# Optimization experiments

Hardware: AMD Instinct MI355X
Metric: run time of the kernel (lower is better)

The kernel has to match this reference:

```python
import jax, jax.numpy as jnp
import numpy as np
import math

A = 256            # n_agents == batch rows (epymarl stacks agents along batch)
B = A
OBS = 512          # obs_shape = (input_shape - n_actions) // 2
NA = 64            # n_actions
MSG = 2048         # messages_shape (divisible by A)
H = 1024           # hidden_dim
T = 3              # trajectory_length
TAU = OBS + NA
VD = MSG // A      # per-agent message dim


def setup_inputs() -> dict:
    key = jax.random.key(0)
    keys = iter(jax.random.split(key, 40))
    def lin(o, i):
        w = jax.random.normal(next(keys), (o, i), jnp.float32) * (i ** -0.5)
        return w, jnp.zeros((o,), jnp.float32)
    d = {}
    d["inputs"] = jax.random.normal(next(keys), (B, 2 * OBS + NA + MSG), jnp.float32)
    d["hidden_state"] = jax.random.normal(next(keys), (B, 3 * H), jnp.float32) * 0.1
    for name, o, i in [("pi_fc1", H, OBS + MSG), ("pi_fc2", NA, H),
                       ("fa_fc1", H, OBS), ("fa_fc2", (A - 1) * NA, H),
                       ("fo_fc1", H, NA * A + OBS), ("fo_fc2", OBS, H),
                       ("am_qs", H, MSG), ("am_ks", H, TAU), ("am_vs", VD, TAU)]:
        d[name + "_w"], d[name + "_b"] = lin(o, i)
    for name in ["pi_rnn", "fa_rnn", "fo_rnn"]:
        d[name + "_wih"], d[name + "_bih"] = lin(3 * H, H)
        d[name + "_whh"], d[name + "_bhh"] = lin(3 * H, H)
    return d


def _gru(x, h, wih, whh, bih, bhh):
    gi = x @ wih.T + bih
    gh = h @ whh.T + bhh
    ir, iz, i_n = jnp.split(gi, 3, -1)
    hr, hz, h_n = jnp.split(gh, 3, -1)
    r = jax.nn.sigmoid(ir + hr)
    z = jax.nn.sigmoid(iz + hz)
    n = jnp.tanh(i_n + r * h_n)
    return (1.0 - z) * n + z * h


def reference(inputs, hidden_state,
              pi_fc1_w, pi_fc1_b, pi_fc2_w, pi_fc2_b,
              pi_rnn_wih, pi_rnn_whh, pi_rnn_bih, pi_rnn_bhh,
              fa_fc1_w, fa_fc1_b, fa_fc2_w, fa_fc2_b,
              fa_rnn_wih, fa_rnn_whh, fa_rnn_bih, fa_rnn_bhh,
              fo_fc1_w, fo_fc1_b, fo_fc2_w, fo_fc2_b,
              fo_rnn_wih, fo_rnn_whh, fo_rnn_bih, fo_rnn_bhh,
              am_qs_w, am_qs_b, am_ks_w, am_ks_b, am_vs_w, am_vs_b):
    sg = jax.lax.stop_gradient
    lin = lambda x, w, b: x @ w.T + b
    h_fa = hidden_state[:, :H]
    h_fo = hidden_state[:, H:2 * H]
    h_pi0 = hidden_state[:, -H:]
    obs = inputs[:, :OBS]
    prev_obs = inputs[:, OBS:2 * OBS]
    prev_act = sg(inputs[:, 2 * OBS:2 * OBS + NA])   # .detach() in torch
    prev_msg = inputs[:, -MSG:]

    def pi(o, m, h):
        x = jax.nn.relu(lin(jnp.concatenate([o, m], -1), pi_fc1_w, pi_fc1_b))
        h2 = _gru(x, h, pi_rnn_wih, pi_rnn_whh, pi_rnn_bih, pi_rnn_bhh)
        return lin(h2, pi_fc2_w, pi_fc2_b), h2

    # ---- ImaginedTrajectory rollout (fixed small T, python loop is structural) ----
    o, a, h_pi = prev_obs, prev_act, h_pi0
    observations, actions = [o], [a]
    for _ in range(T - 1):
        x = jax.nn.relu(lin(o, fa_fc1_w, fa_fc1_b))
        h_fa = _gru(x, h_fa, fa_rnn_wih, fa_rnn_whh, fa_rnn_bih, fa_rnn_bhh)
        q = lin(h_fa, fa_fc2_w, fa_fc2_b)                       # [B,(A-1)*NA]
        qs = jax.nn.softmax(q.reshape(B, A - 1, NA), -1)
        # torch stack(qs_out).reshape(orig): scrambles (A-1,B) order, kept faithfully
        fa = jnp.transpose(qs, (1, 0, 2)).reshape(B, (A - 1) * NA)
        x2 = jax.nn.relu(lin(jnp.concatenate([fa, a, o], -1), fo_fc1_w, fo_fc1_b))
        h_fo = _gru(x2, h_fo, fo_rnn_wih, fo_rnn_whh, fo_rnn_bih, fo_rnn_bhh)
        nxt_o = lin(h_fo, fo_fc2_w, fo_fc2_b)
        nxt_a, h_pi = pi(sg(o), sg(prev_msg), sg(h_pi))         # forward_pi detaches inputs
        o, a = nxt_o, nxt_a
        observations.append(o)
        actions.append(a)
    taus = jnp.stack([jnp.concatenate([observations[t], actions[t]], -1)
                      for t in range(T)])                        # [T,B,TAU]

    # ---- AttentionMechanism: batched equivalent of the per-agent python loops ----
    # k rows are indexed j*n_agents + i with batch == n_agents, i.e. k[t, b] here.
    qv = lin(prev_msg, am_qs_w, am_qs_b)                         # [B,H]
    kk = jnp.einsum('tbi,hi->tbh', taus, am_ks_w) + am_ks_b      # [T,B,H]
    vv = jnp.einsum('tbi,vi->tbv', taus, am_vs_w) + am_vs_b      # [T,B,VD]
    alpha = jax.nn.softmax(jnp.einsum('bh,tbh->bt', qv, kk) / math.sqrt(H), -1)
    new_message = jnp.einsum('bt,tbv->bv', alpha, vv)            # [B,VD]

    # cat([msg]*A, 0).reshape(B,-1): each agent receives all agents' messages
    pi_msg = jnp.tile(new_message, (A, 1)).reshape(B, -1)        # [B,MSG]
    action, h_pi_f = pi(obs, pi_msg, h_pi0)                      # uses ORIGINAL h_pi slice
    h_out = jnp.concatenate([h_fa, h_fo, h_pi_f], -1)            # [B,3H]
    q_out = jnp.concatenate([new_message, action], -1)           # [B,VD+NA]
    return q_out, h_out
```

## Files before the change

### kernel.cpp

```cpp
#include <hip/hip_runtime.h>
#include <hip/hip_bf16.h>
#include <math.h>

#define OBS 512
#define MSG 2048
#define TAU 576
#define TAUP 640
#define QN 16320
#define X2W 16896
#define INW 3136
#define PIW 2560

typedef short short8v __attribute__((ext_vector_type(8)));
typedef float f32x4 __attribute__((ext_vector_type(4)));
typedef __hip_bfloat16 bf;

__device__ inline unsigned short bfbits(float x) {
  bf h = __float2bfloat16(x);
  return *reinterpret_cast<unsigned short*>(&h);
}

__device__ inline ushort4 cvtf4(float4 v) {
  ushort4 r;
  r.x = bfbits(v.x); r.y = bfbits(v.y); r.z = bfbits(v.z); r.w = bfbits(v.w);
  return r;
}

__device__ inline void gload16(const void* g, void* l) {
  __builtin_amdgcn_global_load_lds((__attribute__((address_space(1))) void*)(g),
                                   (__attribute__((address_space(3))) void*)(l), 16, 0, 0);
}

struct MMSet {
  const bf* A;
  const float* W;
  const float* bias;
  float* C;
  bf* Cb;
  int lda, ldw, ldc, ldcb;
};

template<int ACT, bool ATOMIC, bool DUAL>
__global__ __launch_bounds__(256)
void k_mm(MMSet s0, MMSet s1, int kSteps)
{
  __shared__ bf As[2][64 * 64];
  __shared__ bf Bs[2][64 * 64];
  const MMSet S = (DUAL && blockIdx.z) ? s1 : s0;
  const int tid = threadIdx.x;
  const int lane = tid & 63;
  const int wid = tid >> 6;

  const int gx = gridDim.x, gy = gridDim.y;
  const int nwg = gx * gy;
  const int hw = blockIdx.y * gx + blockIdx.x;
  const int qq = nwg >> 3, rr = nwg & 7;
  const int xcd = hw & 7, idx = hw >> 3;
  const int logical = (xcd < rr) ? xcd * (qq + 1) + idx
                                 : rr * (qq + 1) + (xcd - rr) * qq + idx;
  const int m0 = (logical % gy) * 64;
  const int n0 = (logical / gy) * 64;
  const size_t k0 = ATOMIC ? (size_t)blockIdx.z * kSteps * 64 : 0;

  const bf* Ab = S.A + (size_t)m0 * S.lda + k0;
  const float* Bb = S.W + (size_t)n0 * S.ldw + k0;

  int arow[2], acol[2], adst[2];
#pragma unroll
  for (int r = 0; r < 2; ++r) {
    int chunk = r * 256 + tid;
    arow[r] = chunk >> 3;
    acol[r] = ((chunk & 7) ^ (arow[r] & 7)) * 8;
    adst[r] = chunk * 8;
  }
  int brow[4], bcol[4], bdst[4];
#pragma unroll
  for (int r = 0; r < 4; ++r) {
    int c = r * 256 + tid;
    brow[r] = c >> 4;
    int g = (c & 15) >> 1, half = c & 1;
    bcol[r] = (c & 15) * 4;
    bdst[r] = brow[r] * 64 + ((g ^ (brow[r] & 7)) << 3) + half * 4;
  }

  const int wr = wid >> 1, wc = wid & 1;
  const int fr = lane & 15, q = lane >> 4;
  const int xm = fr & 7;

  f32x4 acc00 = {}, acc01 = {}, acc10 = {}, acc11 = {};
  float4 w0, w1, w2, w3;

  auto stageA = [&](int buf, int kt) {
#pragma unroll
    for (int r = 0; r < 2; ++r)
      gload16(Ab + (size_t)arow[r] * S.lda + kt + acol[r], &As[buf][adst[r]]);
  };
  auto loadB = [&](int kt) {
    w0 = *(const float4*)(Bb + (size_t)brow[0] * S.ldw + kt + bcol[0]);
    w1 = *(const float4*)(Bb + (size_t)brow[1] * S.ldw + kt + bcol[1]);
    w2 = *(const float4*)(Bb + (size_t)brow[2] * S.ldw + kt + bcol[2]);
    w3 = *(const float4*)(Bb + (size_t)brow[3] * S.ldw + kt + bcol[3]);
  };
  auto writeB = [&](int buf) {
    *(ushort4*)&Bs[buf][bdst[0]] = cvtf4(w0);
    *(ushort4*)&Bs[buf][bdst[1]] = cvtf4(w1);
    *(ushort4*)&Bs[buf][bdst[2]] = cvtf4(w2);
    *(ushort4*)&Bs[buf][bdst[3]] = cvtf4(w3);
  };

  stageA(0, 0);
  loadB(0);
  writeB(0);
  __syncthreads();

  for (int t = 0; t < kSteps; ++t) {
    const int buf = t & 1;
    if (t + 1 < kSteps) {
      stageA(buf ^ 1, (t + 1) * 64);
      loadB((t + 1) * 64);
    }
    const bf* Ac = As[buf];
    const bf* Bc = Bs[buf];
#pragma unroll
    for (int ks = 0; ks < 2; ++ks) {
      const int cc = ks * 4 + q;
      const int co = ((cc ^ xm) << 3);
      short8v a0 = *(const short8v*)&Ac[(wr * 32 +  0 + fr) * 64 + co];
      short8v a1 = *(const short8v*)&Ac[(wr * 32 + 16 + fr) * 64 + co];
      short8v b0 = *(const short8v*)&Bc[(wc * 32 +  0 + fr) * 64 + co];
      short8v b1 = *(const short8v*)&Bc[(wc * 32 + 16 + fr) * 64 + co];
      acc00 = __builtin_amdgcn_mfma_f32_16x16x32_bf16(a0, b0, acc00, 0, 0, 0);
      acc01 = __builtin_amdgcn_mfma_f32_16x16x32_bf16(a0, b1, acc01, 0, 0, 0);
      acc10 = __builtin_amdgcn_mfma_f32_16x16x32_bf16(a1, b0, acc10, 0, 0, 0);
      acc11 = __builtin_amdgcn_mfma_f32_16x16x32_bf16(a1, b1, acc11, 0, 0, 0);
    }
    if (t + 1 < kSteps) writeB(buf ^ 1);
    __syncthreads();
  }

  const int mb0 = m0 + wr * 32 + q * 4;
  const int mb1 = mb0 + 16;
  const int nc0 = n0 + wc * 32 + fr;
  const int nc1 = nc0 + 16;
  if (ATOMIC) {
#pragma unroll
    for (int v = 0; v < 4; ++v) {
      atomicAdd(&S.C[(size_t)(mb0 + v) * S.ldc + nc0], acc00[v]);
      atomicAdd(&S.C[(size_t)(mb0 + v) * S.ldc + nc1], acc01[v]);
      atomicAdd(&S.C[(size_t)(mb1 + v) * S.ldc + nc0], acc10[v]);
      atomicAdd(&S.C[(size_t)(mb1 + v) * S.ldc + nc1], acc11[v]);
    }
  } else {
    const float bb0 = S.bias[nc0], bb1 = S.bias[nc1];
#pragma unroll
    for (int v = 0; v < 4; ++v) {
      float v00 = acc00[v] + bb0, v01 = acc01[v] + bb1;
      float v10 = acc10[v] + bb0, v11 = acc11[v] + bb1;
      if (ACT) { v00 = fmaxf(v00, 0.f); v01 = fmaxf(v01, 0.f);
                 v10 = fmaxf(v10, 0.f); v11 = fmaxf(v11, 0.f); }
      if (S.C) {
        S.C[(size_t)(mb0 + v) * S.ldc + nc0] = v00;
        S.C[(size_t)(mb0 + v) * S.ldc + nc1] = v01;
        S.C[(size_t)(mb1 + v) * S.ldc + nc0] = v10;
        S.C[(size_t)(mb1 + v) * S.ldc + nc1] = v11;
      }
      if (S.Cb) {
        S.Cb[(size_t)(mb0 + v) * S.ldcb + nc0] = __float2bfloat16(v00);
        S.Cb[(size_t)(mb0 + v) * S.ldcb + nc1] = __float2bfloat16(v01);
        S.Cb[(size_t)(mb1 + v) * S.ldcb + nc0] = __float2bfloat16(v10);
        S.Cb[(size_t)(mb1 + v) * S.ldcb + nc1] = __float2bfloat16(v11);
      }
    }
  }
}

__global__ __launch_bounds__(256)
void k_init(const float* __restrict__ in, const float* __restrict__ hid,
            float* __restrict__ h32a, float* __restrict__ h32o, float* __restrict__ h32p,
            bf* __restrict__ hba, bf* __restrict__ hbo,
            bf* __restrict__ hbp, bf* __restrict__ hbp0,
            bf* __restrict__ taus, bf* __restrict__ msgb,
            const float* __restrict__ fo1b, float* __restrict__ xf0, float* __restrict__ xf1,
            const float* __restrict__ pi1b, float* __restrict__ xp0,
            float* __restrict__ xp1, float* __restrict__ xp2)
{
  const int bx = blockIdx.x;
  if (bx < 3072) {
    int idx = bx * 256 + threadIdx.x;
    int b = idx / 3072, c = idx % 3072;
    float v = hid[idx];
    bf hb = __float2bfloat16(v);
    int j = c & 1023;
    if (c < 1024)      { h32a[b * 1024 + j] = v; hba[b * 1024 + j] = hb; }
    else if (c < 2048) { h32o[b * 1024 + j] = v; hbo[b * 1024 + j] = hb; }
    else               { h32p[b * 1024 + j] = v; hbp[b * 1024 + j] = hb; hbp0[b * 1024 + j] = hb; }
  } else if (bx < 3072 + 1920) {
    int idx = (bx - 3072) * 256 + threadIdx.x;
    int t = idx / (256 * TAUP);
    int r = (idx / TAUP) % 256;
    int c = idx % TAUP;
    float v = 0.f;
    if (t == 0 && c < TAU)
      v = (c < OBS) ? in[(size_t)r * INW + OBS + c]
                    : in[(size_t)r * INW + 2 * OBS + (c - OBS)];
    taus[idx] = __float2bfloat16(v);
  } else if (bx < 3072 + 1920 + 2048) {
    int idx = (bx - 3072 - 1920) * 256 + threadIdx.x;
    int b = idx >> 11, c = idx & 2047;
    msgb[idx] = __float2bfloat16(in[(size_t)b * INW + 1088 + c]);
  } else if (bx < 3072 + 1920 + 2048 + 1024) {
    int idx = (bx - 3072 - 1920 - 2048) * 256 + threadIdx.x;
    float v = fo1b[idx & 1023];
    xf0[idx] = v; xf1[idx] = v;
  } else {
    int idx = (bx - 3072 - 1920 - 2048 - 1024) * 256 + threadIdx.x;
    float v = pi1b[idx & 1023];
    xp0[idx] = v; xp1[idx] = v; xp2[idx] = v;
  }
}

__global__ __launch_bounds__(256)
void k_gru(const float* __restrict__ gi, const float* __restrict__ gh,
           const float* __restrict__ hs, int ldsrc,
           float* __restrict__ hd, int lddst, bf* __restrict__ hb)
{
  int idx = blockIdx.x * 256 + threadIdx.x;
  int b = idx >> 10, j = idx & 1023;
  float ir = gi[b * 3072 + j];
  float iz = gi[b * 3072 + 1024 + j];
  float in_ = gi[b * 3072 + 2048 + j];
  float hr = gh[b * 3072 + j];
  float hz = gh[b * 3072 + 1024 + j];
  float hn = gh[b * 3072 + 2048 + j];
  float r = 1.f / (1.f + expf(-(ir + hr)));
  float z = 1.f / (1.f + expf(-(iz + hz)));
  float n = tanhf(in_ + r * hn);
  float h = hs[(size_t)b * ldsrc + j];
  float o = (1.f - z) * n + z * h;
  hd[(size_t)b * lddst + j] = o;
  hb[idx] = __float2bfloat16(o);
}

__global__ __launch_bounds__(256)
void k_softmax_scatter(const bf* __restrict__ q, bf* __restrict__ x2)
{
  int wid = blockIdx.x * 4 + (threadIdx.x >> 6);
  int lane = threadIdx.x & 63;
  int b = wid / 255, p = wid % 255;
  float v = __bfloat162float(q[(size_t)b * QN + p * 64 + lane]);
  float m = v;
#pragma unroll
  for (int s = 32; s; s >>= 1) m = fmaxf(m, __shfl_xor(m, s));
  float e = expf(v - m);
  float sum = e;
#pragma unroll
  for (int s = 32; s; s >>= 1) sum += __shfl_xor(sum, s);
  float r = e / sum;
  int flat = p * 16384 + b * 64 + lane;
  int bp = flat / QN;
  int j = flat - bp * QN;
  x2[(size_t)bp * X2W + j] = __float2bfloat16(r);
}

__global__ __launch_bounds__(256)
void k_x2_tail(const bf* __restrict__ taus_t, bf* __restrict__ x2)
{
  int idx = blockIdx.x * 256 + threadIdx.x;
  int b = idx / TAU, c = idx % TAU;
  if (c < 64)
    x2[(size_t)b * X2W + QN + c] = taus_t[(size_t)b * TAUP + OBS + c];
  else
    x2[(size_t)b * X2W + QN + 64 + (c - 64)] = taus_t[(size_t)b * TAUP + (c - 64)];
}

__global__ __launch_bounds__(256)
void k_concat_pi_loop(const bf* __restrict__ taus_t, const bf* __restrict__ msg,
                      bf* __restrict__ piin)
{
  int idx = blockIdx.x * 256 + threadIdx.x;
  int b = idx / PIW, c = idx % PIW;
  piin[idx] = (c < OBS) ? taus_t[(size_t)b * TAUP + c] : msg[b * MSG + (c - OBS)];
}

__global__ __launch_bounds__(256)
void k_concat_pi_final(const float* __restrict__ in, const float* __restrict__ nm,
                       bf* __restrict__ piin)
{
  int idx = blockIdx.x * 256 + threadIdx.x;
  int b = idx / PIW, c = idx % PIW;
  float v = (c < OBS) ? in[(size_t)b * INW + c] : nm[c - OBS];
  piin[idx] = __float2bfloat16(v);
}

__global__ __launch_bounds__(256)
void k_relu_cvt(const float* __restrict__ s, bf* __restrict__ d)
{
  int idx = blockIdx.x * 256 + threadIdx.x;
  d[idx] = __float2bfloat16(fmaxf(s[idx], 0.f));
}

__global__ __launch_bounds__(64)
void k_vv(const bf* __restrict__ taus, const float* __restrict__ w,
          const float* __restrict__ bias, float* __restrict__ vv)
{
  int row = blockIdx.x;
  int lane = threadIdx.x;
  const bf* tr = taus + (size_t)row * TAUP;
  for (int v = 0; v < 8; ++v) {
    float s = 0.f;
    for (int k = lane; k < TAU; k += 64) s += __bfloat162float(tr[k]) * w[v * TAU + k];
#pragma unroll
    for (int d = 32; d; d >>= 1) s += __shfl_xor(s, d);
    if (lane == 0) vv[row * 8 + v] = s + bias[v];
  }
}

__global__ __launch_bounds__(64)
void k_attn(const float* __restrict__ qv, const float* __restrict__ kk,
            const float* __restrict__ vv, float* __restrict__ nm,
            float* __restrict__ out_q)
{
  int b = blockIdx.x;
  int lane = threadIdx.x;
  const float* qb = qv + (size_t)b * 1024;
  float s[3];
#pragma unroll
  for (int t = 0; t < 3; ++t) {
    const float* kb = kk + (size_t)(t * 256 + b) * 1024;
    float acc = 0.f;
    for (int h = lane; h < 1024; h += 64) acc += qb[h] * kb[h];
#pragma unroll
    for (int d = 32; d; d >>= 1) acc += __shfl_xor(acc, d);
    s[t] = acc * (1.f / 32.f);
  }
  float m = fmaxf(s[0], fmaxf(s[1], s[2]));
  float e0 = expf(s[0] - m), e1 = expf(s[1] - m), e2 = expf(s[2] - m);
  float inv = 1.f / (e0 + e1 + e2);
  float a0 = e0 * inv, a1 = e1 * inv, a2 = e2 * inv;
  if (lane < 8) {
    float v = a0 * vv[(0 * 256 + b) * 8 + lane]
            + a1 * vv[(1 * 256 + b) * 8 + lane]
            + a2 * vv[(2 * 256 + b) * 8 + lane];
    nm[b * 8 + lane] = v;
    out_q[b * 72 + lane] = v;
  }
}

__global__ __launch_bounds__(256)
void k_copy_hout(const float* __restrict__ hfa, const float* __restrict__ hfo,
                 float* __restrict__ hout)
{
  int idx = blockIdx.x * 256 + threadIdx.x;
  int b = idx / 2048, c = idx % 2048;
  float v = (c < 1024) ? hfa[b * 1024 + c] : hfo[b * 1024 + (c - 1024)];
  hout[(size_t)b * 3072 + c] = v;
}

extern "C" void kernel_launch(void* const* d_in, const int* in_sizes, int n_in,
                              void* d_out_v, int out_size, void* d_ws, size_t ws_size,
                              hipStream_t stream)
{
  const float* inputs   = (const float*)d_in[0];
  const float* hidden   = (const float*)d_in[1];
  const float* pi_fc1_w = (const float*)d_in[2];
  const float* pi_fc1_b = (const float*)d_in[3];
  const float* pi_fc2_w = (const float*)d_in[4];
  const float* pi_fc2_b = (const float*)d_in[5];
  const float* fa_fc1_w = (const float*)d_in[6];
  const float* fa_fc1_b = (const float*)d_in[7];
  const float* fa_fc2_w = (const float*)d_in[8];
  const float* fa_fc2_b = (const float*)d_in[9];
  const float* fo_fc1_w = (const float*)d_in[10];
  const float* fo_fc1_b = (const float*)d_in[11];
  const float* fo_fc2_w = (const float*)d_in[12];
  const float* fo_fc2_b = (const float*)d_in[13];
  const float* am_qs_w  = (const float*)d_in[14];
  const float* am_qs_b  = (const float*)d_in[15];
  const float* am_ks_w  = (const float*)d_in[16];
  const float* am_ks_b  = (const float*)d_in[17];
  const float* am_vs_w  = (const float*)d_in[18];
  const float* am_vs_b  = (const float*)d_in[19];
  const float* pi_wih   = (const float*)d_in[20];
  const float* pi_bih   = (const float*)d_in[21];
  const float* pi_whh   = (const float*)d_in[22];
  const float* pi_bhh   = (const float*)d_in[23];
  const float* fa_wih   = (const float*)d_in[24];
  const float* fa_bih   = (const float*)d_in[25];
  const float* fa_whh   = (const float*)d_in[26];
  const float* fa_bhh   = (const float*)d_in[27];
  const float* fo_wih   = (const float*)d_in[28];
  const float* fo_bih   = (const float*)d_in[29];
  const float* fo_whh   = (const float*)d_in[30];
  const float* fo_bhh   = (const float*)d_in[31];

  float* out = (float*)d_out_v;
  char* p = (char*)d_ws;
  auto alloc = [&](size_t bytes) { void* r = p; p += (bytes + 255) & ~(size_t)255; return r; };

  bf* HFAB = (bf*)alloc((size_t)256 * 1024 * 2);
  bf* HFOB = (bf*)alloc((size_t)256 * 1024 * 2);
  bf* HPIB = (bf*)alloc((size_t)256 * 1024 * 2);
  bf* HPI0B = (bf*)alloc((size_t)256 * 1024 * 2);
  bf* XBUFB = (bf*)alloc((size_t)256 * 1024 * 2);
  bf* TAUSB = (bf*)alloc((size_t)3 * 256 * TAUP * 2);
  bf* X2B  = (bf*)alloc((size_t)256 * X2W * 2);
  bf* PIINB = (bf*)alloc((size_t)256 * PIW * 2);
  bf* MSGB = (bf*)alloc((size_t)256 * MSG * 2);
  bf* QBUFB = (bf*)alloc((size_t)256 * QN * 2);
  float* HFA32 = (float*)alloc((size_t)256 * 1024 * 4);
  float* HFO32 = (float*)alloc((size_t)256 * 1024 * 4);
  float* HPI32 = (float*)alloc((size_t)256 * 1024 * 4);
  float* XF32A = (float*)alloc((size_t)256 * 1024 * 4);
  float* XF32B = (float*)alloc((size_t)256 * 1024 * 4);
  float* XP32A = (float*)alloc((size_t)256 * 1024 * 4);
  float* XP32B = (float*)alloc((size_t)256 * 1024 * 4);
  float* XP32C = (float*)alloc((size_t)256 * 1024 * 4);
  float* GI = (float*)alloc((size_t)256 * 3072 * 4);
  float* GH = (float*)alloc((size_t)256 * 3072 * 4);
  float* QV = (float*)alloc((size_t)256 * 1024 * 4);
  float* KK = (float*)alloc((size_t)768 * 1024 * 4);
  float* VV = (float*)alloc((size_t)768 * 8 * 4);
  float* NM = (float*)alloc((size_t)2048 * 4);

  auto mset = [&](const bf* A, int lda, const float* W, int ldw, const float* bias,
                  float* C, int ldc, bf* Cb, int ldcb) {
    MMSet s; s.A = A; s.W = W; s.bias = bias; s.C = C; s.Cb = Cb;
    s.lda = lda; s.ldw = ldw; s.ldc = ldc; s.ldcb = ldcb; return s;
  };
  auto mm = [&](MMSet a, int M, int N, int K, int act) {
    dim3 g(N / 64, M / 64, 1);
    if (act) k_mm<1, false, false><<<g, 256, 0, stream>>>(a, a, K / 64);
    else     k_mm<0, false, false><<<g, 256, 0, stream>>>(a, a, K / 64);
  };
  auto mmAtomic = [&](const bf* A, int lda, const float* W, int ldw,
                      float* C, int M, int N, int K, int z) {
    MMSet s = mset(A, lda, W, ldw, nullptr, C, N, nullptr, 0);
    dim3 g(N / 64, M / 64, z);
    k_mm<0, true, false><<<g, 256, 0, stream>>>(s, s, K / (64 * z));
  };
  auto mmDual = [&](MMSet a, MMSet b, int N, int K) {
    dim3 g(N / 64, 4, 2);
    k_mm<0, false, true><<<g, 256, 0, stream>>>(a, b, K / 64);
  };

  k_init<<<3072 + 1920 + 2048 + 1024 + 1024, 256, 0, stream>>>(inputs, hidden,
      HFA32, HFO32, HPI32, HFAB, HFOB, HPIB, HPI0B, TAUSB, MSGB,
      fo_fc1_b, XF32A, XF32B, pi_fc1_b, XP32A, XP32B, XP32C);

  for (int t = 0; t < 2; ++t) {
    bf* taus_t = TAUSB + (size_t)t * 256 * TAUP;
    bf* taus_n = TAUSB + (size_t)(t + 1) * 256 * TAUP;
    float* xf32 = t ? XF32B : XF32A;
    float* xp32 = t ? XP32B : XP32A;
    mm(mset(taus_t, TAUP, fa_fc1_w, 512, fa_fc1_b, nullptr, 0, XBUFB, 1024), 256, 1024, 512, 1);
    mmDual(mset(XBUFB, 1024, fa_wih, 1024, fa_bih, GI, 3072, nullptr, 0),
           mset(HFAB, 1024, fa_whh, 1024, fa_bhh, GH, 3072, nullptr, 0), 3072, 1024);
    k_gru<<<1024, 256, 0, stream>>>(GI, GH, HFA32, 1024, HFA32, 1024, HFAB);
    mm(mset(HFAB, 1024, fa_fc2_w, 1024, fa_fc2_b, nullptr, 0, QBUFB, QN), 256, QN, 1024, 0);
    k_x2_tail<<<576, 256, 0, stream>>>(taus_t, X2B);
    k_softmax_scatter<<<16320, 256, 0, stream>>>(QBUFB, X2B);
    mmAtomic(X2B, X2W, fo_fc1_w, X2W, xf32, 256, 1024, X2W, 12);
    k_relu_cvt<<<1024, 256, 0, stream>>>(xf32, XBUFB);
    mmDual(mset(XBUFB, 1024, fo_wih, 1024, fo_bih, GI, 3072, nullptr, 0),
           mset(HFOB, 1024, fo_whh, 1024, fo_bhh, GH, 3072, nullptr, 0), 3072, 1024);
    k_gru<<<1024, 256, 0, stream>>>(GI, GH, HFO32, 1024, HFO32, 1024, HFOB);
    mm(mset(HFOB, 1024, fo_fc2_w, 1024, fo_fc2_b, nullptr, 0, taus_n, TAUP), 256, 512, 1024, 0);
    k_concat_pi_loop<<<2560, 256, 0, stream>>>(taus_t, MSGB, PIINB);
    mmAtomic(PIINB, PIW, pi_fc1_w, PIW, xp32, 256, 1024, PIW, 4);
    k_relu_cvt<<<1024, 256, 0, stream>>>(xp32, XBUFB);
    mmDual(mset(XBUFB, 1024, pi_wih, 1024, pi_bih, GI, 3072, nullptr, 0),
           mset(HPIB, 1024, pi_whh, 1024, pi_bhh, GH, 3072, nullptr, 0), 3072, 1024);
    k_gru<<<1024, 256, 0, stream>>>(GI, GH, HPI32, 1024, HPI32, 1024, HPIB);
    mm(mset(HPIB, 1024, pi_fc2_w, 1024, pi_fc2_b, nullptr, 0, taus_n + OBS, TAUP), 256, 64, 1024, 0);
  }

  mm(mset(MSGB, MSG, am_qs_w, MSG, am_qs_b, QV, 1024, nullptr, 0), 256, 1024, 2048, 0);
  mm(mset(TAUSB, TAUP, am_ks_w, TAU, am_ks_b, KK, 1024, nullptr, 0), 768, 1024, TAU, 0);
  k_vv<<<768, 64, 0, stream>>>(TAUSB, am_vs_w, am_vs_b, VV);
  k_attn<<<256, 64, 0, stream>>>(QV, KK, VV, NM, out);

  k_concat_pi_final<<<2560, 256, 0, stream>>>(inputs, NM, PIINB);
  mmAtomic(PIINB, PIW, pi_fc1_w, PIW, XP32C, 256, 1024, PIW, 4);
  k_relu_cvt<<<1024, 256, 0, stream>>>(XP32C, XBUFB);
  mmDual(mset(XBUFB, 1024, pi_wih, 1024, pi_bih, GI, 3072, nullptr, 0),
         mset(HPI0B, 1024, pi_whh, 1024, pi_bhh, GH, 3072, nullptr, 0), 3072, 1024);
  k_gru<<<1024, 256, 0, stream>>>(GI, GH, hidden + 2048, 3072,
                                  out + 256 * 72 + 2048, 3072, HPIB);
  mm(mset(HPIB, 1024, pi_fc2_w, 1024, pi_fc2_b, out + 8, 72, nullptr, 0), 256, 64, 1024, 0);
  k_copy_hout<<<2048, 256, 0, stream>>>(HFA32, HFO32, out + 256 * 72);
  (void)in_sizes; (void)n_in; (void)out_size; (void)ws_size;
}
```

Before: 617.6 us.

## Stage B weights in 256-wide K macro-tiles with deeper load prefetch

Adds a MACRO variant of the bf16 MFMA GEMM in which each block loads a 64x256 fp32 weight slab into registers (16 float4 per thread), converts it to bf16 and stores it in LDS once per four 64-wide K steps. The A operand stays double-buffered per 64-step. The aim is more weight loads in flight per thread, to hide global latency on these weight-bandwidth-bound GEMMs. Split-K counts for the atomic GEMMs are changed (12 to 11, 4 to 5) to fit the 256 granularity. The keys GEMM (K=576) stays on the old path. The costs are extra syncthreads per step, higher register pressure and a larger LDS footprint.

```diff
diff --git a/kernel.cpp b/kernel.cpp
--- a/kernel.cpp
+++ b/kernel.cpp
@@ -40,12 +40,13 @@
   int lda, ldw, ldc, ldcb;
 };
 
-template<int ACT, bool ATOMIC, bool DUAL>
+template<int ACT, bool ATOMIC, bool DUAL, bool MACRO>
 __global__ __launch_bounds__(256)
 void k_mm(MMSet s0, MMSet s1, int kSteps)
 {
+  constexpr int BSN = MACRO ? (64 * 256) : (2 * 64 * 64);
   __shared__ bf As[2][64 * 64];
-  __shared__ bf Bs[2][64 * 64];
+  __shared__ bf Bs[BSN];
   const MMSet S = (DUAL && blockIdx.z) ? s1 : s0;
   const int tid = threadIdx.x;
   const int lane = tid & 63;
@@ -60,7 +61,7 @@
                                  : rr * (qq + 1) + (xcd - rr) * qq + idx;
   const int m0 = (logical % gy) * 64;
   const int n0 = (logical / gy) * 64;
-  const size_t k0 = ATOMIC ? (size_t)blockIdx.z * kSteps * 64 : 0;
+  const size_t k0 = ATOMIC ? (size_t)blockIdx.z * kSteps * (MACRO ? 256 : 64) : 0;
 
   const bf* Ab = S.A + (size_t)m0 * S.lda + k0;
   const float* Bb = S.W + (size_t)n0 * S.ldw + k0;
@@ -73,69 +74,121 @@
     acol[r] = ((chunk & 7) ^ (arow[r] & 7)) * 8;
     adst[r] = chunk * 8;
   }
-  int brow[4], bcol[4], bdst[4];
-#pragma unroll
-  for (int r = 0; r < 4; ++r) {
-    int c = r * 256 + tid;
-    brow[r] = c >> 4;
-    int g = (c & 15) >> 1, half = c & 1;
-    bcol[r] = (c & 15) * 4;
-    bdst[r] = brow[r] * 64 + ((g ^ (brow[r] & 7)) << 3) + half * 4;
-  }
-
   const int wr = wid >> 1, wc = wid & 1;
   const int fr = lane & 15, q = lane >> 4;
   const int xm = fr & 7;
 
   f32x4 acc00 = {}, acc01 = {}, acc10 = {}, acc11 = {};
-  float4 w0, w1, w2, w3;
 
   auto stageA = [&](int buf, int kt) {
 #pragma unroll
     for (int r = 0; r < 2; ++r)
       gload16(Ab + (size_t)arow[r] * S.lda + kt + acol[r], &As[buf][adst[r]]);
   };
-  auto loadB = [&](int kt) {
-    w0 = *(const float4*)(Bb + (size_t)brow[0] * S.ldw + kt + bcol[0]);
-    w1 = *(const float4*)(Bb + (size_t)brow[1] * S.ldw + kt + bcol[1]);
-    w2 = *(const float4*)(Bb + (size_t)brow[2] * S.ldw + kt + bcol[2]);
-    w3 = *(const float4*)(Bb + (size_t)brow[3] * S.ldw + kt + bcol[3]);
-  };
-  auto writeB = [&](int buf) {
-    *(ushort4*)&Bs[buf][bdst[0]] = cvtf4(w0);
-    *(ushort4*)&Bs[buf][bdst[1]] = cvtf4(w1);
-    *(ushort4*)&Bs[buf][bdst[2]] = cvtf4(w2);
-    *(ushort4*)&Bs[buf][bdst[3]] = cvtf4(w3);
-  };
-
-  stageA(0, 0);
-  loadB(0);
-  writeB(0);
-  __syncthreads();
-
-  for (int t = 0; t < kSteps; ++t) {
-    const int buf = t & 1;
-    if (t + 1 < kSteps) {
-      stageA(buf ^ 1, (t + 1) * 64);
-      loadB((t + 1) * 64);
+
+  const int ar0 = wr * 32 + fr, ar1 = ar0 + 16;
+  const int br0 = wc * 32 + fr, br1 = br0 + 16;
+
+  if constexpr (MACRO) {
+    float4 wreg[16];
+    const int rw = tid >> 6;
+    const int lb = tid & 63;
+    const int gB = lb >> 1, hB = lb & 1;
+    const int subB = gB >> 3, gloB = gB & 7;
+    auto loadB = [&](int mi) {
+      const float* base = Bb + (size_t)mi * 256 + lb * 4;
+#pragma unroll
+      for (int j = 0; j < 16; ++j)
+        wreg[j] = *(const float4*)(base + (size_t)(j * 4 + rw) * S.ldw);
+    };
+    auto writeB = [&]() {
+#pragma unroll
+      for (int j = 0; j < 16; ++j) {
+        const int r = j * 4 + rw;
+        const int off = r * 256 + (subB * 8 + (gloB ^ (r & 7))) * 8 + hB * 4;
+        *(ushort4*)&Bs[off] = cvtf4(wreg[j]);
+      }
+    };
+    loadB(0);
+    writeB();
+    stageA(0, 0);
+    __syncthreads();
+    const int total = kSteps * 4;
+    for (int m = 0; m < kSteps; ++m) {
+      if (m + 1 < kSteps) loadB(m + 1);
+#pragma unroll
+      for (int s = 0; s < 4; ++s) {
+        const int u = m * 4 + s;
+        if (u + 1 < total) stageA((u + 1) & 1, (u + 1) * 64);
+        const bf* Ac = As[u & 1];
+#pragma unroll
+        for (int ks = 0; ks < 2; ++ks) {
+          const int cc = ks * 4 + q;
+          const int co = ((cc ^ xm) << 3);
+          short8v a0 = *(const short8v*)&Ac[ar0 * 64 + co];
+          short8v a1 = *(const short8v*)&Ac[ar1 * 64 + co];
+          short8v b0 = *(const short8v*)&Bs[br0 * 256 + s * 64 + co];
+          short8v b1 = *(const short8v*)&Bs[br1 * 256 + s * 64 + co];
+          acc00 = __builtin_amdgcn_mfma_f32_16x16x32_bf16(a0, b0, acc00, 0, 0, 0);
+          acc01 = __builtin_amdgcn_mfma_f32_16x16x32_bf16(a0, b1, acc01, 0, 0, 0);
+          acc10 = __builtin_amdgcn_mfma_f32_16x16x32_bf16(a1, b0, acc10, 0, 0, 0);
+          acc11 = __builtin_amdgcn_mfma_f32_16x16x32_bf16(a1, b1, acc11, 0, 0, 0);
+        }
+        __syncthreads();
+      }
+      if (m + 1 < kSteps) { writeB(); __syncthreads(); }
     }
-    const bf* Ac = As[buf];
-    const bf* Bc = Bs[buf];
-#pragma unroll
-    for (int ks = 0; ks < 2; ++ks) {
-      const int cc = ks * 4 + q;
-      const int co = ((cc ^ xm) << 3);
-      short8v a0 = *(const short8v*)&Ac[(wr * 32 +  0 + fr) * 64 + co];
-      short8v a1 = *(const short8v*)&Ac[(wr * 32 + 16 + fr) * 64 + co];
-      short8v b0 = *(const short8v*)&Bc[(wc * 32 +  0 + fr) * 64 + co];
-      short8v b1 = *(const short8v*)&Bc[(wc * 32 + 16 + fr) * 64 + co];
-      acc00 = __builtin_amdgcn_mfma_f32_16x16x32_bf16(a0, b0, acc00, 0, 0, 0);
-      acc01 = __builtin_amdgcn_mfma_f32_16x16x32_bf16(a0, b1, acc01, 0, 0, 0);
-      acc10 = __builtin_amdgcn_mfma_f32_16x16x32_bf16(a1, b0, acc10, 0, 0, 0);
-      acc11 = __builtin_amdgcn_mfma_f32_16x16x32_bf16(a1, b1, acc11, 0, 0, 0);
+  } else {
+    int brow[4], bcol[4], bdst[4];
+#pragma unroll
+    for (int r = 0; r < 4; ++r) {
+      int c = r * 256 + tid;
+      brow[r] = c >> 4;
+      int g = (c & 15) >> 1, half = c & 1;
+      bcol[r] = (c & 15) * 4;
+      bdst[r] = brow[r] * 64 + ((g ^ (brow[r] & 7)) << 3) + half * 4;
     }
-    if (t + 1 < kSteps) writeB(buf ^ 1);
+    float4 w0, w1, w2, w3;
+    auto loadB = [&](int kt) {
+      w0 = *(const float4*)(Bb + (size_t)brow[0] * S.ldw + kt + bcol[0]);
+      w1 = *(const float4*)(Bb + (size_t)brow[1] * S.ldw + kt + bcol[1]);
+      w2 = *(const float4*)(Bb + (size_t)brow[2] * S.ldw + kt + bcol[2]);
+      w3 = *(const float4*)(Bb + (size_t)brow[3] * S.ldw + kt + bcol[3]);
+    };
+    auto writeB = [&](int buf) {
+      *(ushort4*)&Bs[buf * 4096 + bdst[0]] = cvtf4(w0);
+      *(ushort4*)&Bs[buf * 4096 + bdst[1]] = cvtf4(w1);
+      *(ushort4*)&Bs[buf * 4096 + bdst[2]] = cvtf4(w2);
+      *(ushort4*)&Bs[buf * 4096 + bdst[3]] = cvtf4(w3);
+    };
+    stageA(0, 0);
+    loadB(0);
+    writeB(0);
     __syncthreads();
+    for (int t = 0; t < kSteps; ++t) {
+      const int buf = t & 1;
+      if (t + 1 < kSteps) {
+        stageA(buf ^ 1, (t + 1) * 64);
+        loadB((t + 1) * 64);
+      }
+      const bf* Ac = As[buf];
+      const bf* Bc = &Bs[buf * 4096];
+#pragma unroll
+      for (int ks = 0; ks < 2; ++ks) {
+        const int cc = ks * 4 + q;
+        const int co = ((cc ^ xm) << 3);
+        short8v a0 = *(const short8v*)&Ac[ar0 * 64 + co];
+        short8v a1 = *(const short8v*)&Ac[ar1 * 64 + co];
+        short8v b0 = *(const short8v*)&Bc[br0 * 64 + co];
+        short8v b1 = *(const short8v*)&Bc[br1 * 64 + co];
+        acc00 = __builtin_amdgcn_mfma_f32_16x16x32_bf16(a0, b0, acc00, 0, 0, 0);
+        acc01 = __builtin_amdgcn_mfma_f32_16x16x32_bf16(a0, b1, acc01, 0, 0, 0);
+        acc10 = __builtin_amdgcn_mfma_f32_16x16x32_bf16(a1, b0, acc10, 0, 0, 0);
+        acc11 = __builtin_amdgcn_mfma_f32_16x16x32_bf16(a1, b1, acc11, 0, 0, 0);
+      }
+      if (t + 1 < kSteps) writeB(buf ^ 1);
+      __syncthreads();
+    }
   }
 
   const int mb0 = m0 + wr * 32 + q * 4;
@@ -427,20 +480,24 @@
     MMSet s; s.A = A; s.W = W; s.bias = bias; s.C = C; s.Cb = Cb;
     s.lda = lda; s.ldw = ldw; s.ldc = ldc; s.ldcb = ldcb; return s;
   };
-  auto mm = [&](MMSet a, int M, int N, int K, int act) {
+  auto mmM = [&](MMSet a, int M, int N, int K, int act) {
     dim3 g(N / 64, M / 64, 1);
-    if (act) k_mm<1, false, false><<<g, 256, 0, stream>>>(a, a, K / 64);
-    else     k_mm<0, false, false><<<g, 256, 0, stream>>>(a, a, K / 64);
+    if (act) k_mm<1, false, false, true><<<g, 256, 0, stream>>>(a, a, K / 256);
+    else     k_mm<0, false, false, true><<<g, 256, 0, stream>>>(a, a, K / 256);
   };
-  auto mmAtomic = [&](const bf* A, int lda, const float* W, int ldw,
-                      float* C, int M, int N, int K, int z) {
+  auto mmAtomicM = [&](const bf* A, int lda, const float* W, int ldw,
+                       float* C, int M, int N, int K, int z) {
     MMSet s = mset(A, lda, W, ldw, nullptr, C, N, nullptr, 0);
     dim3 g(N / 64, M / 64, z);
-    k_mm<0, true, false><<<g, 256, 0, stream>>>(s, s, K / (64 * z));
+    k_mm<0, true, false, true><<<g, 256, 0, stream>>>(s, s, K / (256 * z));
   };
-  auto mmDual = [&](MMSet a, MMSet b, int N, int K) {
+  auto mmDualM = [&](MMSet a, MMSet b, int N, int K) {
     dim3 g(N / 64, 4, 2);
-    k_mm<0, false, true><<<g, 256, 0, stream>>>(a, b, K / 64);
+    k_mm<0, false, true, true><<<g, 256, 0, stream>>>(a, b, K / 256);
+  };
+  auto mmKS = [&](MMSet a, int M, int N, int K) {
+    dim3 g(N / 64, M / 64, 1);
+    k_mm<0, false, false, false><<<g, 256, 0, stream>>>(a, a, K / 64);
   };
 
   k_init<<<3072 + 1920 + 2048 + 1024 + 1024, 256, 0, stream>>>(inputs, hidden,
@@ -452,41 +509,41 @@
     bf* taus_n = TAUSB + (size_t)(t + 1) * 256 * TAUP;
     float* xf32 = t ? XF32B : XF32A;
     float* xp32 = t ? XP32B : XP32A;
-    mm(mset(taus_t, TAUP, fa_fc1_w, 512, fa_fc1_b, nullptr, 0, XBUFB, 1024), 256, 1024, 512, 1);
-    mmDual(mset(XBUFB, 1024, fa_wih, 1024, fa_bih, GI, 3072, nullptr, 0),
-           mset(HFAB, 1024, fa_whh, 1024, fa_bhh, GH, 3072, nullptr, 0), 3072, 1024);
+    mmM(mset(taus_t, TAUP, fa_fc1_w, 512, fa_fc1_b, nullptr, 0, XBUFB, 1024), 256, 1024, 512, 1);
+    mmDualM(mset(XBUFB, 1024, fa_wih, 1024, fa_bih, GI, 3072, nullptr, 0),
+            mset(HFAB, 1024, fa_whh, 1024, fa_bhh, GH, 3072, nullptr, 0), 3072, 1024);
     k_gru<<<1024, 256, 0, stream>>>(GI, GH, HFA32, 1024, HFA32, 1024, HFAB);
-    mm(mset(HFAB, 1024, fa_fc2_w, 1024, fa_fc2_b, nullptr, 0, QBUFB, QN), 256, QN, 1024, 0);
+    mmM(mset(HFAB, 1024, fa_fc2_w, 1024, fa_fc2_b, nullptr, 0, QBUFB, QN), 256, QN, 1024, 0);
     k_x2_tail<<<576, 256, 0, stream>>>(taus_t, X2B);
     k_softmax_scatter<<<16320, 256, 0, stream>>>(QBUFB, X2B);
-    mmAtomic(X2B, X2W, fo_fc1_w, X2W, xf32, 256, 1024, X2W, 12);
+    mmAtomicM(X2B, X2W, fo_fc1_w, X2W, xf32, 256, 1024, X2W, 11);
     k_relu_cvt<<<1024, 256, 0, stream>>>(xf32, XBUFB);
-    mmDual(mset(XBUFB, 1024, fo_wih, 1024, fo_bih, GI, 3072, nullptr, 0),
-           mset(HFOB, 1024, fo_whh, 1024, fo_bhh, GH, 3072, nullptr, 0), 3072, 1024);
+    mmDualM(mset(XBUFB, 1024, fo_wih, 1024, fo_bih, GI, 3072, nullptr, 0),
+            mset(HFOB, 1024, fo_whh, 1024, fo_bhh, GH, 3072, nullptr, 0), 3072, 1024);
     k_gru<<<1024, 256, 0, stream>>>(GI, GH, HFO32, 1024, HFO32, 1024, HFOB);
-    mm(mset(HFOB, 1024, fo_fc2_w, 1024, fo_fc2_b, nullptr, 0, taus_n, TAUP), 256, 512, 1024, 0);
+    mmM(mset(HFOB, 1024, fo_fc2_w, 1024, fo_fc2_b, nullptr, 0, taus_n, TAUP), 256, 512, 1024, 0);
     k_concat_pi_loop<<<2560, 256, 0, stream>>>(taus_t, MSGB, PIINB);
-    mmAtomic(PIINB, PIW, pi_fc1_w, PIW, xp32, 256, 1024, PIW, 4);
+    mmAtomicM(PIINB, PIW, pi_fc1_w, PIW, xp32, 256, 1024, PIW, 5);
     k_relu_cvt<<<1024, 256, 0, stream>>>(xp32, XBUFB);
-    mmDual(mset(XBUFB, 1024, pi_wih, 1024, pi_bih, GI, 3072, nullptr, 0),
-           mset(HPIB, 1024, pi_whh, 1024, pi_bhh, GH, 3072, nullptr, 0), 3072, 1024);
+    mmDualM(mset(XBUFB, 1024, pi_wih, 1024, pi_bih, GI, 3072, nullptr, 0),
+            mset(HPIB, 1024, pi_whh, 1024, pi_bhh, GH, 3072, nullptr, 0), 3072, 1024);
     k_gru<<<1024, 256, 0, stream>>>(GI, GH, HPI32, 1024, HPI32, 1024, HPIB);
-    mm(mset(HPIB, 1024, pi_fc2_w, 1024, pi_fc2_b, nullptr, 0, taus_n + OBS, TAUP), 256, 64, 1024, 0);
-  }
-
-  mm(mset(MSGB, MSG, am_qs_w, MSG, am_qs_b, QV, 1024, nullptr, 0), 256, 1024, 2048, 0);
-  mm(mset(TAUSB, TAUP, am_ks_w, TAU, am_ks_b, KK, 1024, nullptr, 0), 768, 1024, TAU, 0);
+    mmM(mset(HPIB, 1024, pi_fc2_w, 1024, pi_fc2_b, nullptr, 0, taus_n + OBS, TAUP), 256, 64, 1024, 0);
+  }
+
+  mmM(mset(MSGB, MSG, am_qs_w, MSG, am_qs_b, QV, 1024, nullptr, 0), 256, 1024, 2048, 0);
+  mmKS(mset(TAUSB, TAUP, am_ks_w, TAU, am_ks_b, KK, 1024, nullptr, 0), 768, 1024, 576);
   k_vv<<<768, 64, 0, stream>>>(TAUSB, am_vs_w, am_vs_b, VV);
   k_attn<<<256, 64, 0, stream>>>(QV, KK, VV, NM, out);
 
   k_concat_pi_final<<<2560, 256, 0, stream>>>(inputs, NM, PIINB);
-  mmAtomic(PIINB, PIW, pi_fc1_w, PIW, XP32C, 256, 1024, PIW, 4);
+  mmAtomicM(PIINB, PIW, pi_fc1_w, PIW, XP32C, 256, 1024, PIW, 5);
   k_relu_cvt<<<1024, 256, 0, stream>>>(XP32C, XBUFB);
-  mmDual(mset(XBUFB, 1024, pi_wih, 1024, pi_bih, GI, 3072, nullptr, 0),
-         mset(HPI0B, 1024, pi_whh, 1024, pi_bhh, GH, 3072, nullptr, 0), 3072, 1024);
+  mmDualM(mset(XBUFB, 1024, pi_wih, 1024, pi_bih, GI, 3072, nullptr, 0),
+          mset(HPI0B, 1024, pi_whh, 1024, pi_bhh, GH, 3072, nullptr, 0), 3072, 1024);
   k_gru<<<1024, 256, 0, stream>>>(GI, GH, hidden + 2048, 3072,
                                   out + 256 * 72 + 2048, 3072, HPIB);
-  mm(mset(HPIB, 1024, pi_fc2_w, 1024, pi_fc2_b, out + 8, 72, nullptr, 0), 256, 64, 1024, 0);
+  mmM(mset(HPIB, 1024, pi_fc2_w, 1024, pi_fc2_b, out + 8, 72, nullptr, 0), 256, 64, 1024, 0);
   k_copy_hout<<<2048, 256, 0, stream>>>(HFA32, HFO32, out + 256 * 72);
   (void)in_sizes; (void)n_in; (void)out_size; (void)ws_size;
 }
```

Result: no change. 628.1 us (+1.7%).

## Add full-M 256x128 GEMM kernel for fp32-weight layers so weights stream once

Applied to the files above, without the earlier changes.

Adds a new 512-thread GEMM kernel whose block covers all 256 rows and 128 columns, so each fp32 weight row is loaded and converted to bf16 only once rather than once per 64-row M tile. The large fa_fc2, fo_fc1 and pi_fc1 projections use it, with split-K atomics for the fc1 layers; fo_fc1 split changed from 12 to 8. The am_qs projection moves to the start as a split-K atomic GEMM, with its bias preloaded in the init kernel. Tradeoff: fewer blocks, so lower parallelism on skinny layers, and higher register and LDS use per block.

```diff
diff --git a/kernel.cpp b/kernel.cpp
--- a/kernel.cpp
+++ b/kernel.cpp
@@ -174,6 +174,117 @@
   }
 }
 
+template<int ACT, bool ATOMIC>
+__global__ __launch_bounds__(512)
+void k_mm2(MMSet S, int kSteps, int Nw, int Nlim)
+{
+  __shared__ bf As[2][256 * 32];
+  __shared__ bf Bs[2][128 * 32];
+  const int tid = threadIdx.x;
+  const int lane = tid & 63;
+  const int wid = tid >> 6;
+  const int n0 = blockIdx.x * 128;
+  const size_t k0 = (size_t)blockIdx.z * kSteps * 32;
+
+  const bf* Ab = S.A + k0;
+
+  int arow[2], acol[2], adst[2];
+#pragma unroll
+  for (int r = 0; r < 2; ++r) {
+    int c = r * 512 + tid;
+    arow[r] = c >> 2;
+    acol[r] = ((c & 3) ^ (arow[r] & 3)) * 8;
+    adst[r] = c * 8;
+  }
+  const float* bsrc[2];
+  int bdst[2];
+#pragma unroll
+  for (int r = 0; r < 2; ++r) {
+    int c = r * 512 + tid;
+    int row = c >> 3, f4 = c & 7;
+    int rowg = n0 + row; if (rowg >= Nw) rowg = Nw - 1;
+    bsrc[r] = S.W + (size_t)rowg * S.ldw + k0 + f4 * 4;
+    bdst[r] = row * 32 + (((f4 >> 1) ^ (row & 3)) << 3) + (f4 & 1) * 4;
+  }
+
+  const int wr = wid & 3, wc = wid >> 2;
+  const int fr = lane & 15, q = lane >> 4;
+
+  f32x4 acc[4][4] = {};
+  float4 w0, w1;
+
+  auto stageA = [&](int buf, int kt) {
+#pragma unroll
+    for (int r = 0; r < 2; ++r)
+      gload16(Ab + (size_t)arow[r] * S.lda + kt + acol[r], &As[buf][adst[r]]);
+  };
+  auto loadB = [&](int kt) {
+    w0 = *(const float4*)(bsrc[0] + kt);
+    w1 = *(const float4*)(bsrc[1] + kt);
+  };
+  auto writeB = [&](int buf) {
+    *(ushort4*)&Bs[buf][bdst[0]] = cvtf4(w0);
+    *(ushort4*)&Bs[buf][bdst[1]] = cvtf4(w1);
+  };
+
+  stageA(0, 0);
+  loadB(0);
+  writeB(0);
+  __syncthreads();
+
+  for (int t = 0; t < kSteps; ++t) {
+    const int buf = t & 1;
+    if (t + 1 < kSteps) {
+      stageA(buf ^ 1, (t + 1) * 32);
+      loadB((t + 1) * 32);
+    }
+    const bf* Ac = As[buf];
+    const bf* Bc = Bs[buf];
+    short8v af[4], bfv[4];
+#pragma unroll
+    for (int i = 0; i < 4; ++i) {
+      const int ar = wr * 64 + i * 16 + fr;
+      af[i] = *(const short8v*)&Ac[ar * 32 + ((q ^ (ar & 3)) << 3)];
+    }
+#pragma unroll
+    for (int j = 0; j < 4; ++j) {
+      const int br = wc * 64 + j * 16 + fr;
+      bfv[j] = *(const short8v*)&Bc[br * 32 + ((q ^ (br & 3)) << 3)];
+    }
+#pragma unroll
+    for (int i = 0; i < 4; ++i)
+#pragma unroll
+      for (int j = 0; j < 4; ++j)
+        acc[i][j] = __builtin_amdgcn_mfma_f32_16x16x32_bf16(af[i], bfv[j], acc[i][j], 0, 0, 0);
+    if (t + 1 < kSteps) writeB(buf ^ 1);
+    __syncthreads();
+  }
+
+#pragma unroll
+  for (int i = 0; i < 4; ++i) {
+    const int mb = wr * 64 + i * 16 + q * 4;
+#pragma unroll
+    for (int j = 0; j < 4; ++j) {
+      const int n = n0 + wc * 64 + j * 16 + fr;
+      if (n >= Nlim) continue;
+      if (ATOMIC) {
+#pragma unroll
+        for (int v = 0; v < 4; ++v)
+          atomicAdd(&S.C[(size_t)(mb + v) * S.ldc + n], acc[i][j][v]);
+      } else {
+        const float bb = S.bias[n];
+#pragma unroll
+        for (int v = 0; v < 4; ++v) {
+          float val = acc[i][j][v] + bb;
+          if (ACT) val = fmaxf(val, 0.f);
+          if (S.C)  S.C[(size_t)(mb + v) * S.ldc + n] = val;
+          if (S.Cb) S.Cb[(size_t)(mb + v) * S.ldcb + n] = __float2bfloat16(val);
+        }
+      }
+    }
+  }
+}
+
 __global__ __launch_bounds__(256)
 void k_init(const float* __restrict__ in, const float* __restrict__ hid,
             float* __restrict__ h32a, float* __restrict__ h32o, float* __restrict__ h32p,
@@ -182,7 +293,8 @@
             bf* __restrict__ taus, bf* __restrict__ msgb,
             const float* __restrict__ fo1b, float* __restrict__ xf0, float* __restrict__ xf1,
             const float* __restrict__ pi1b, float* __restrict__ xp0,
-            float* __restrict__ xp1, float* __restrict__ xp2)
+            float* __restrict__ xp1, float* __restrict__ xp2,
+            const float* __restrict__ qsb, float* __restrict__ qv)
 {
   const int bx = blockIdx.x;
   if (bx < 3072) {
@@ -212,10 +324,13 @@
     int idx = (bx - 3072 - 1920 - 2048) * 256 + threadIdx.x;
     float v = fo1b[idx & 1023];
     xf0[idx] = v; xf1[idx] = v;
-  } else {
+  } else if (bx < 3072 + 1920 + 2048 + 2048) {
     int idx = (bx - 3072 - 1920 - 2048 - 1024) * 256 + threadIdx.x;
     float v = pi1b[idx & 1023];
     xp0[idx] = v; xp1[idx] = v; xp2[idx] = v;
+  } else {
+    int idx = (bx - 3072 - 1920 - 2048 - 2048) * 256 + threadIdx.x;
+    qv[idx] = qsb[idx & 1023];
   }
 }
 
@@ -432,20 +547,26 @@
     if (act) k_mm<1, false, false><<<g, 256, 0, stream>>>(a, a, K / 64);
     else     k_mm<0, false, false><<<g, 256, 0, stream>>>(a, a, K / 64);
   };
-  auto mmAtomic = [&](const bf* A, int lda, const float* W, int ldw,
-                      float* C, int M, int N, int K, int z) {
-    MMSet s = mset(A, lda, W, ldw, nullptr, C, N, nullptr, 0);
-    dim3 g(N / 64, M / 64, z);
-    k_mm<0, true, false><<<g, 256, 0, stream>>>(s, s, K / (64 * z));
-  };
   auto mmDual = [&](MMSet a, MMSet b, int N, int K) {
     dim3 g(N / 64, 4, 2);
     k_mm<0, false, true><<<g, 256, 0, stream>>>(a, b, K / 64);
   };
-
-  k_init<<<3072 + 1920 + 2048 + 1024 + 1024, 256, 0, stream>>>(inputs, hidden,
+  auto mm2 = [&](MMSet a, int Npad, int Nw, int Nlim, int K) {
+    dim3 g(Npad / 128, 1, 1);
+    k_mm2<0, false><<<g, 512, 0, stream>>>(a, K / 32, Nw, Nlim);
+  };
+  auto mm2Atomic = [&](const bf* A, int lda, const float* W, int ldw,
+                       float* C, int N, int K, int z) {
+    MMSet s = mset(A, lda, W, ldw, nullptr, C, N, nullptr, 0);
+    dim3 g(N / 128, 1, z);
+    k_mm2<0, true><<<g, 512, 0, stream>>>(s, K / (32 * z), N, N);
+  };
+
+  k_init<<<3072 + 1920 + 2048 + 1024 + 1024 + 1024, 256, 0, stream>>>(inputs, hidden,
       HFA32, HFO32, HPI32, HFAB, HFOB, HPIB, HPI0B, TAUSB, MSGB,
-      fo_fc1_b, XF32A, XF32B, pi_fc1_b, XP32A, XP32B, XP32C);
+      fo_fc1_b, XF32A, XF32B, pi_fc1_b, XP32A, XP32B, XP32C, am_qs_b, QV);
+
+  mm2Atomic(MSGB, MSG, am_qs_w, MSG, QV, 1024, 2048, 2);
 
   for (int t = 0; t < 2; ++t) {
     bf* taus_t = TAUSB + (size_t)t * 256 * TAUP;
@@ -456,17 +577,18 @@
     mmDual(mset(XBUFB, 1024, fa_wih, 1024, fa_bih, GI, 3072, nullptr, 0),
            mset(HFAB, 1024, fa_whh, 1024, fa_bhh, GH, 3072, nullptr, 0), 3072, 1024);
     k_gru<<<1024, 256, 0, stream>>>(GI, GH, HFA32, 1024, HFA32, 1024, HFAB);
-    mm(mset(HFAB, 1024, fa_fc2_w, 1024, fa_fc2_b, nullptr, 0, QBUFB, QN), 256, QN, 1024, 0);
+    mm2(mset(HFAB, 1024, fa_fc2_w, 1024, fa_fc2_b, nullptr, 0, QBUFB, QN),
+        16384, QN, QN, 1024);
     k_x2_tail<<<576, 256, 0, stream>>>(taus_t, X2B);
     k_softmax_scatter<<<16320, 256, 0, stream>>>(QBUFB, X2B);
-    mmAtomic(X2B, X2W, fo_fc1_w, X2W, xf32, 256, 1024, X2W, 12);
+    mm2Atomic(X2B, X2W, fo_fc1_w, X2W, xf32, 1024, X2W, 8);
     k_relu_cvt<<<1024, 256, 0, stream>>>(xf32, XBUFB);
     mmDual(mset(XBUFB, 1024, fo_wih, 1024, fo_bih, GI, 3072, nullptr, 0),
            mset(HFOB, 1024, fo_whh, 1024, fo_bhh, GH, 3072, nullptr, 0), 3072, 1024);
     k_gru<<<1024, 256, 0, stream>>>(GI, GH, HFO32, 1024, HFO32, 1024, HFOB);
     mm(mset(HFOB, 1024, fo_fc2_w, 1024, fo_fc2_b, nullptr, 0, taus_n, TAUP), 256, 512, 1024, 0);
     k_concat_pi_loop<<<2560, 256, 0, stream>>>(taus_t, MSGB, PIINB);
-    mmAtomic(PIINB, PIW, pi_fc1_w, PIW, xp32, 256, 1024, PIW, 4);
+    mm2Atomic(PIINB, PIW, pi_fc1_w, PIW, xp32, 1024, PIW, 4);
     k_relu_cvt<<<1024, 256, 0, stream>>>(xp32, XBUFB);
     mmDual(mset(XBUFB, 1024, pi_wih, 1024, pi_bih, GI, 3072, nullptr, 0),
            mset(HPIB, 1024, pi_whh, 1024, pi_bhh, GH, 3072, nullptr, 0), 3072, 1024);
@@ -474,13 +596,12 @@
     mm(mset(HPIB, 1024, pi_fc2_w, 1024, pi_fc2_b, nullptr, 0, taus_n + OBS, TAUP), 256, 64, 1024, 0);
   }
 
-  mm(mset(MSGB, MSG, am_qs_w, MSG, am_qs_b, QV, 1024, nullptr, 0), 256, 1024, 2048, 0);
   mm(mset(TAUSB, TAUP, am_ks_w, TAU, am_ks_b, KK, 1024, nullptr, 0), 768, 1024, TAU, 0);
   k_vv<<<768, 64, 0, stream>>>(TAUSB, am_vs_w, am_vs_b, VV);
   k_attn<<<256, 64, 0, stream>>>(QV, KK, VV, NM, out);
 
   k_concat_pi_final<<<2560, 256, 0, stream>>>(inputs, NM, PIINB);
-  mmAtomic(PIINB, PIW, pi_fc1_w, PIW, XP32C, 256, 1024, PIW, 4);
+  mm2Atomic(PIINB, PIW, pi_fc1_w, PIW, XP32C, 1024, PIW, 4);
   k_relu_cvt<<<1024, 256, 0, stream>>>(XP32C, XBUFB);
   mmDual(mset(XBUFB, 1024, pi_wih, 1024, pi_bih, GI, 3072, nullptr, 0),
          mset(HPI0B, 1024, pi_whh, 1024, pi_bhh, GH, 3072, nullptr, 0), 3072, 1024);
```

After: 824.8 us. 1.34x slower.
